# Kernel optimization log

Measured on AMD Instinct MI355X. Metric: run time of the kernel, lower is better.

Reference implementation:

```python
import jax, jax.numpy as jnp
import numpy as np

B, S, A, H, Z = 256, 512, 64, 1024, 256

def setup_inputs() -> dict:
    key = jax.random.key(0)
    ks = jax.random.split(key, 24)
    w = lambda k, shape: (jax.random.normal(k, shape, jnp.float32) * 0.02)
    inp = {
        "x": jax.random.randint(ks[0], (B, S), 0, A),
        "h0": jax.random.normal(ks[1], (B, H), jnp.float32),            # init_hidden randn
        "eps": jax.random.normal(ks[2], (S + 1, B, Z), jnp.float32),     # reparam noise per step + final
        "phi_x_w": w(ks[3], (H, A)),  "phi_x_b": jnp.zeros((H,), jnp.float32),
        "enc_w1": w(ks[4], (H, 2 * H)), "enc_b1": jnp.zeros((H,), jnp.float32),
        "enc_w2": w(ks[5], (Z, H)),     "enc_b2": jnp.zeros((Z,), jnp.float32),
        "pri_w1": w(ks[6], (H, H)),     "pri_b1": jnp.zeros((H,), jnp.float32),
        "pri_w2": w(ks[7], (Z, H)),     "pri_b2": jnp.zeros((Z,), jnp.float32),
        "phi_z_w": w(ks[8], (H, Z)),    "phi_z_b": jnp.zeros((H,), jnp.float32),
        "dec_w": w(ks[9], (H, 2 * H)),  "dec_b": jnp.zeros((H,), jnp.float32),
        "act_w": w(ks[10], (A, H)),     "act_b": jnp.zeros((A,), jnp.float32),
        "gru_wih": w(ks[11], (3 * H, 2 * H)), "gru_whh": w(ks[12], (3 * H, H)),
        "gru_bih": jnp.zeros((3 * H,), jnp.float32), "gru_bhh": jnp.zeros((3 * H,), jnp.float32),
    }
    return inp

def reference(x, h0, eps, phi_x_w, phi_x_b, enc_w1, enc_b1, enc_w2, enc_b2,
              pri_w1, pri_b1, pri_w2, pri_b2, phi_z_w, phi_z_b, dec_w, dec_b,
              act_w, act_b, gru_wih, gru_whh, gru_bih, gru_bhh):
    relu, sp = jax.nn.relu, jax.nn.softplus

    def gru_cell(xin, h):  # PyTorch GRU gate math
        gi = xin @ gru_wih.T + gru_bih
        gh = h @ gru_whh.T + gru_bhh
        ir, iz, inn = jnp.split(gi, 3, axis=-1)
        hr, hz, hn = jnp.split(gh, 3, axis=-1)
        r = jax.nn.sigmoid(ir + hr)
        zg = jax.nn.sigmoid(iz + hz)
        n = jnp.tanh(inn + r * hn)
        return (1.0 - zg) * n + zg * h

    def prior(h):
        p = relu(h @ pri_w1.T + pri_b1) @ pri_w2.T + pri_b2
        return p, sp(p)

    x_oh = jax.nn.one_hot(x, A, dtype=jnp.float32).transpose(1, 0, 2)  # [S,B,A]

    def step(carry, inp):
        h, kld = carry
        x_t, eps_t = inp
        px = relu(x_t @ phi_x_w.T + phi_x_b)                            # [B,H]
        enc = relu(jnp.concatenate([px, h], -1) @ enc_w1.T + enc_b1) @ enc_w2.T + enc_b2
        enc_std = sp(enc)
        pri_m, pri_std = prior(h)
        kld_el = (2 * jnp.log(pri_std) - 2 * jnp.log(enc_std)
                  + (enc_std ** 2 + (enc - pri_m) ** 2) / pri_std ** 2 - 1.0)
        kld = kld + 0.5 * jnp.sum(kld_el)
        z_t = eps_t * enc_std + enc                                     # reparam sample
        pz = relu(z_t @ phi_z_w.T + phi_z_b)
        h_new = gru_cell(jnp.concatenate([px, pz], -1), h)
        return (h_new, kld), None

    (h, kld), _ = jax.lax.scan(step, (h0, jnp.float32(0.0)), (x_oh, eps[:S]))

    pri_m, pri_std = prior(h)
    z_t = eps[S] * pri_std + pri_m
    pz = relu(z_t @ phi_z_w.T + phi_z_b)
    dec = relu(jnp.concatenate([pz, h], -1) @ dec_w.T + dec_b)
    pred_act = dec @ act_w.T + act_b
    return pred_act, kld
```

## Files before the change

### kernel.cpp

```cpp
#include <hip/hip_runtime.h>


typedef float f32x4 __attribute__((ext_vector_type(4)));
typedef __bf16 bf16x8 __attribute__((ext_vector_type(8)));
typedef unsigned long long u64;
typedef u64 u64x2 __attribute__((ext_vector_type(2)));

#define BB 256
#define SS 512
#define HH 1024
#define ZZ 256
#define AA 64
#define NWG 256

__device__ __forceinline__ float softplus_(float x) {
    return (x > 15.f) ? x : log1pf(expf(x));
}
__device__ __forceinline__ float sigmoid_(float x) {
    return 1.f / (1.f + expf(-x));
}

__device__ __forceinline__ u64 ld8a(const __bf16* p) {
    return __hip_atomic_load((const u64*)p, __ATOMIC_RELAXED, __HIP_MEMORY_SCOPE_AGENT);
}
__device__ __forceinline__ bf16x8 ld16a(const __bf16* p) {
    u64x2 t; t.x = ld8a(p); t.y = ld8a(p + 4);
    return __builtin_bit_cast(bf16x8, t);
}
__device__ __forceinline__ void st2a(__bf16* p, float v) {
    unsigned w = __builtin_bit_cast(unsigned short, (__bf16)v);
    asm volatile("global_store_short %0, %1, off sc0 sc1" :: "v"(p), "v"(w) : "memory");
}

__device__ __forceinline__ void gbarR(unsigned* bar, unsigned p, int wg) {
    __syncthreads();
    if (threadIdx.x == 0) {
        unsigned s = p & 7u;
        unsigned exp = (p >> 3) + 1u;
        unsigned* leaf = bar + (s * 8 + (wg >> 5)) * 16;
        unsigned* root = bar + (64 + s) * 16;
        unsigned* flag = bar + (72 + s) * 16;
        unsigned old = __hip_atomic_fetch_add(leaf, 1u, __ATOMIC_RELAXED, __HIP_MEMORY_SCOPE_AGENT);
        if (old == 32u * exp - 1u) {
            unsigned old2 = __hip_atomic_fetch_add(root, 1u, __ATOMIC_RELAXED, __HIP_MEMORY_SCOPE_AGENT);
            if (old2 == 8u * exp - 1u)
                __hip_atomic_store(flag, exp, __ATOMIC_RELAXED, __HIP_MEMORY_SCOPE_AGENT);
        }
        while (__hip_atomic_load(flag, __ATOMIC_RELAXED, __HIP_MEMORY_SCOPE_AGENT) < exp)
            __builtin_amdgcn_s_sleep(2);
    }
    asm volatile("buffer_inv sc0" ::: "memory");
    __syncthreads();
}

__device__ __forceinline__ void xbar(unsigned* flags, int g, int rank, int ngrp,
                                     unsigned tok) {
    __syncthreads();
    if (threadIdx.x == 0)
        __hip_atomic_store(flags + g * 256 + rank, tok, __ATOMIC_RELAXED,
                           __HIP_MEMORY_SCOPE_AGENT);
    unsigned l = threadIdx.x & 63;
    unsigned* base = flags + g * 256;
    for (;;) {
        bool ok = true;
        for (int i = (int)l; i < ngrp; i += 64)
            ok &= (__hip_atomic_load(base + i, __ATOMIC_RELAXED,
                                     __HIP_MEMORY_SCOPE_AGENT) >= tok);
        if (__all(ok)) break;
        __builtin_amdgcn_s_sleep(2);
    }
    asm volatile("buffer_inv sc0" ::: "memory");
    __syncthreads();
}

template<int MT, int NT>
__device__ __forceinline__ void wgemm(const __bf16* __restrict__ A, int lda, int mstride,
                                      const __bf16* __restrict__ B, int ldb, int nstride,
                                      int K, f32x4 (&acc)[MT][NT]) {
    int lane = threadIdx.x & 63;
    int rr = lane & 15;
    int ko = (lane >> 4) * 8;
    const __bf16* ap = A + rr * lda + ko;
    const __bf16* bp = B + rr * ldb + ko;
    #pragma unroll 2
    for (int k = 0; k < K; k += 32) {
        bf16x8 af[MT], bfr[NT];
        #pragma unroll
        for (int mt = 0; mt < MT; mt++) af[mt] = *(const bf16x8*)(ap + mt * mstride + k);
        #pragma unroll
        for (int nt = 0; nt < NT; nt++) bfr[nt] = *(const bf16x8*)(bp + nt * nstride + k);
        #pragma unroll
        for (int mt = 0; mt < MT; mt++)
            #pragma unroll
            for (int nt = 0; nt < NT; nt++)
                acc[mt][nt] = __builtin_amdgcn_mfma_f32_16x16x32_bf16(af[mt], bfr[nt], acc[mt][nt], 0, 0, 0);
    }
}


__global__ void k_zeroctl(unsigned* bar, unsigned* flags, unsigned* cnt, float* kldacc) {
    for (int i = threadIdx.x; i < 1280; i += 256) bar[i] = 0u;
    for (int i = threadIdx.x; i < 2048; i += 256) flags[i] = 0u;
    if (threadIdx.x < 8) cnt[threadIdx.x] = 0u;
    if (threadIdx.x == 0) *kldacc = 0.f;
}

__global__ void k_pack(const float* __restrict__ src, int src_ld, int col_off,
                       __bf16* __restrict__ dst, int cols, int total) {
    int i = blockIdx.x * 256 + threadIdx.x;
    if (i >= total) return;
    int r = i / cols, c = i - r * cols;
    dst[i] = (__bf16)src[r * src_ld + col_off + c];
}

__global__ void k_copyf(const float* __restrict__ s, float* __restrict__ d, int n) {
    int i = blockIdx.x * 256 + threadIdx.x;
    if (i < n) d[i] = s[i];
}

__global__ void k_px(const float* __restrict__ phi_x_w, const float* __restrict__ phi_x_b,
                     float* __restrict__ px) {
    int i = blockIdx.x * 256 + threadIdx.x;
    int a = i >> 10, hh = i & 1023;
    px[i] = fmaxf(phi_x_w[hh * AA + a] + phi_x_b[hh], 0.f);
}

__global__ __launch_bounds__(256) void k_tables(const float* __restrict__ enc_w1,
                                                const float* __restrict__ wih,
                                                const float* __restrict__ px,
                                                float* __restrict__ encpx,
                                                float* __restrict__ gipx) {
    __shared__ float spx[64][65];
    int tid = threadIdx.x;
    int cg = blockIdx.x * 4 + (tid >> 6);
    int a = tid & 63;
    const float* wrow = (cg < 1024) ? (enc_w1 + cg * 2048) : (wih + (cg - 1024) * 2048);
    float sum = 0.f;
    for (int k0 = 0; k0 < 1024; k0 += 64) {
        __syncthreads();
        for (int e = tid; e < 4096; e += 256)
            spx[e >> 6][e & 63] = px[((e >> 6) << 10) + k0 + (e & 63)];
        __syncthreads();
        #pragma unroll 8
        for (int kk = 0; kk < 64; kk++) sum += wrow[k0 + kk] * spx[a][kk];
    }
    if (cg < 1024) encpx[a * 1024 + cg] = sum;
    else gipx[a * 3072 + (cg - 1024)] = sum;
}


struct PArgs {
    const int* x; const float* eps;
    const __bf16 *WA, *W2, *WPZ, *WIH, *WHH, *WDEC, *WACT;
    const float *encpx, *gipx;
    const float *eb1, *pb1, *eb2, *pb2, *pzb, *decb, *actb, *bih, *bhh;
    float *hf0, *hf1; __bf16 *hb0, *hb1;
    __bf16 *hidcat, *zbuf, *pzbuf, *tailhid, *decbuf;
    float *gh; float *kldacc; unsigned *bar, *flags, *cnt;
    float* out;
};

__global__ __launch_bounds__(256, 1) void k_persist(PArgs a) {
    int wg = blockIdx.x;
    int tid = threadIdx.x;
    int v = tid >> 6;
    int lane = tid & 63;
    int rr = lane & 15;
    int ko = (lane >> 4) * 8;
    int col = lane & 15, rq = (lane >> 4) * 4;
    float kl = 0.f;
    float* hf[2] = {a.hf0, a.hf1};
    __bf16* hb[2] = {a.hb0, a.hb1};

    __shared__ __align__(16) __bf16 Alds[16][1032];
    __shared__ float lds2[4][2][256];
    __shared__ int sh_g, sh_rank, sh_ngrp;
    __shared__ float sh_kl[4];

    if (tid == 0) {
        unsigned xcc = __builtin_amdgcn_s_getreg((31 << 11) | (0 << 6) | 20) & 7u;
        sh_g = (int)xcc;
        sh_rank = (int)atomicAdd(a.cnt + xcc, 1u);
    }
    __syncthreads();
    int g = sh_g, rank = sh_rank;
    gbarR(a.bar, 0, wg);
    if (tid == 0)
        sh_ngrp = (int)__hip_atomic_load(a.cnt + g, __ATOMIC_RELAXED,
                                         __HIP_MEMORY_SCOPE_AGENT);
    __syncthreads();
    int ngrp = sh_ngrp;
    int base_m = g * 32;

    unsigned gp = 1;

    for (int t = 0; t < SS; t++) {
        int cur = t & 1, nxt = cur ^ 1;

        for (int r0 = rank; r0 < 32; r0 += ngrp) {
            int mt = r0 & 15;
            __syncthreads();
            {
                const __bf16* src = hb[cur] + (size_t)(mt * 16) * HH + tid * 4;
                u64 tmp[16];
                #pragma unroll
                for (int e2 = 0; e2 < 16; e2++) tmp[e2] = ld8a(src + (size_t)e2 * HH);
                #pragma unroll
                for (int e2 = 0; e2 < 16; e2++)
                    *(u64*)((char*)(&Alds[e2][0]) + tid * 8) = tmp[e2];
            }
            __syncthreads();
            int ntg = (r0 >> 4) + 2 * v;
            const __bf16* bp[5]; int qv[5];
            #pragma unroll
            for (int j = 0; j < 5; j++) {
                int q = ntg * 5 + j; qv[j] = q;
                const __bf16* b;
                if (q < 16) b = a.WA + (size_t)(g * 256 + q * 16 + rr) * HH;
                else {
                    int qq = q - 16;
                    b = a.WHH + (size_t)((qq >> 3) * 1024 + g * 128 + (qq & 7) * 16 + rr) * HH;
                }
                bp[j] = b + ko;
            }
            f32x4 acc[5] = {};
            const __bf16* arow = &Alds[rr][ko];
            #pragma unroll 4
            for (int k = 0; k < HH; k += 32) {
                bf16x8 af = *(const bf16x8*)(arow + k);
                #pragma unroll
                for (int j = 0; j < 5; j++)
                    acc[j] = __builtin_amdgcn_mfma_f32_16x16x32_bf16(
                        af, *(const bf16x8*)(bp[j] + k), acc[j], 0, 0, 0);
            }
            int xb[4];
            #pragma unroll
            for (int i = 0; i < 4; i++) xb[i] = a.x[(mt * 16 + rq + i) * SS + t];
            #pragma unroll
            for (int j = 0; j < 5; j++) {
                int q = qv[j];
                if (q < 16) {
                    int c = g * 256 + q * 16 + col;
                    if (c < 1024) {
                        float bias = a.eb1[c];
                        #pragma unroll
                        for (int i = 0; i < 4; i++) {
                            int m = mt * 16 + rq + i;
                            float val = acc[j][i] + bias + a.encpx[xb[i] * 1024 + c];
                            st2a(&a.hidcat[(size_t)m * 2048 + c], fmaxf(val, 0.f));
                        }
                    } else {
                        float bias = a.pb1[c - 1024];
                        #pragma unroll
                        for (int i = 0; i < 4; i++) {
                            int m = mt * 16 + rq + i;
                            st2a(&a.hidcat[(size_t)m * 2048 + c], fmaxf(acc[j][i] + bias, 0.f));
                        }
                    }
                } else {
                    int qq = q - 16;
                    int gc = (qq >> 3) * 1024 + g * 128 + (qq & 7) * 16 + col;
                    #pragma unroll
                    for (int i = 0; i < 4; i++)
                        a.gh[(size_t)(mt * 16 + rq + i) * 3072 + gc] = acc[j][i];
                }
            }
        }
        gbarR(a.bar, gp++, wg);

        for (int r = rank; r < 32; r += ngrp) {
            int mtl = r >> 1;
            int zsl = g * 2 + (r & 1);
            const __bf16* ae_p = a.hidcat + (size_t)(mtl * 16 + rr) * 2048 + v * 256 + ko;
            const __bf16* ap_p = ae_p + 1024;
            const __bf16* be_p = a.W2 + (size_t)(zsl * 16 + rr) * HH + v * 256 + ko;
            const __bf16* bp_p = a.W2 + (size_t)(256 + zsl * 16 + rr) * HH + v * 256 + ko;
            bf16x8 aef[8], apf[8];
            #pragma unroll
            for (int k8 = 0; k8 < 8; k8++) {
                aef[k8] = ld16a(ae_p + k8 * 32);
                apf[k8] = ld16a(ap_p + k8 * 32);
            }
            f32x4 ae = {0.f,0.f,0.f,0.f}, av = {0.f,0.f,0.f,0.f};
            #pragma unroll
            for (int k8 = 0; k8 < 8; k8++) {
                ae = __builtin_amdgcn_mfma_f32_16x16x32_bf16(
                    aef[k8], *(const bf16x8*)(be_p + k8 * 32), ae, 0, 0, 0);
                av = __builtin_amdgcn_mfma_f32_16x16x32_bf16(
                    apf[k8], *(const bf16x8*)(bp_p + k8 * 32), av, 0, 0, 0);
            }
            #pragma unroll
            for (int i = 0; i < 4; i++) {
                int idx = (rq + i) * 16 + col;
                lds2[v][0][idx] = ae[i];
                lds2[v][1][idx] = av[i];
            }
            __syncthreads();
            {
                float e = lds2[0][0][tid] + lds2[1][0][tid] + lds2[2][0][tid] + lds2[3][0][tid];
                float pv = lds2[0][1][tid] + lds2[1][1][tid] + lds2[2][1][tid] + lds2[3][1][tid];
                int m = mtl * 16 + (tid >> 4);
                int z = zsl * 16 + (tid & 15);
                float enc = e + a.eb2[z];
                float pri = pv + a.pb2[z];
                float es = softplus_(enc), ps = softplus_(pri);
                float d = enc - pri;
                kl += 2.f * (logf(ps) - logf(es)) + (es * es + d * d) / (ps * ps) - 1.f;
                const float* epst = a.eps + (size_t)t * BB * ZZ;
                st2a(&a.zbuf[(size_t)m * ZZ + z], epst[m * ZZ + z] * es + enc);
            }
            __syncthreads();
        }
        gbarR(a.bar, gp++, wg);

        for (int r0 = rank; r0 < 32; r0 += ngrp) {
            int mt = r0 & 15;
            int nt = (r0 >> 4) + 2 * v;
            const __bf16* apz = a.zbuf + (size_t)(mt * 16 + rr) * ZZ + ko;
            const __bf16* bpz = a.WPZ + (size_t)((g * 8 + nt) * 16 + rr) * ZZ + ko;
            bf16x8 azf[8];
            #pragma unroll
            for (int k8 = 0; k8 < 8; k8++) azf[k8] = ld16a(apz + k8 * 32);
            f32x4 acc = {0.f,0.f,0.f,0.f};
            #pragma unroll
            for (int k8 = 0; k8 < 8; k8++)
                acc = __builtin_amdgcn_mfma_f32_16x16x32_bf16(
                    azf[k8], *(const bf16x8*)(bpz + k8 * 32), acc, 0, 0, 0);
            int n = (g * 8 + nt) * 16 + col;
            float b = a.pzb[n];
            #pragma unroll
            for (int i = 0; i < 4; i++)
                st2a(&a.pzbuf[(size_t)(mt * 16 + rq + i) * HH + n], fmaxf(acc[i] + b, 0.f));
        }
        gbarR(a.bar, gp++, wg);

        for (int r0 = rank; r0 < 32; r0 += ngrp) {
            int mt = r0 & 15;
            __syncthreads();
            {
                const __bf16* src = a.pzbuf + (size_t)(mt * 16) * HH + tid * 4;
                u64 tmp[16];
                #pragma unroll
                for (int e2 = 0; e2 < 16; e2++) tmp[e2] = ld8a(src + (size_t)e2 * HH);
                #pragma unroll
                for (int e2 = 0; e2 < 16; e2++)
                    *(u64*)((char*)(&Alds[e2][0]) + tid * 8) = tmp[e2];
            }
            __syncthreads();
            int jt = (r0 >> 4) + 2 * v;
            int jtg = g * 8 + jt;
            const __bf16* bp0 = a.WIH + (size_t)(jtg * 16 + rr) * HH + ko;
            const __bf16* bp1g = bp0 + (size_t)1024 * HH;
            const __bf16* bp2g = bp0 + (size_t)2048 * HH;
            f32x4 acc[3] = {};
            const __bf16* arow = &Alds[rr][ko];
            #pragma unroll 4
            for (int k = 0; k < HH; k += 32) {
                bf16x8 af = *(const bf16x8*)(arow + k);
                acc[0] = __builtin_amdgcn_mfma_f32_16x16x32_bf16(af, *(const bf16x8*)(bp0 + k), acc[0], 0, 0, 0);
                acc[1] = __builtin_amdgcn_mfma_f32_16x16x32_bf16(af, *(const bf16x8*)(bp1g + k), acc[1], 0, 0, 0);
                acc[2] = __builtin_amdgcn_mfma_f32_16x16x32_bf16(af, *(const bf16x8*)(bp2g + k), acc[2], 0, 0, 0);
            }
            int j = jtg * 16 + col;
            float br = a.bih[j], bz2 = a.bih[1024 + j], bn = a.bih[2048 + j];
            float cr = a.bhh[j], cz = a.bhh[1024 + j], cn = a.bhh[2048 + j];
            #pragma unroll
            for (int i = 0; i < 4; i++) {
                int m = mt * 16 + rq + i;
                int xb = a.x[m * SS + t];
                const float* gpp = a.gipx + (size_t)xb * 3072;
                const float* ghrow = a.gh + (size_t)m * 3072;
                float gir = acc[0][i] + gpp[j] + br;
                float giz = acc[1][i] + gpp[1024 + j] + bz2;
                float gin = acc[2][i] + gpp[2048 + j] + bn;
                float ghr = ghrow[j] + cr;
                float ghz = ghrow[1024 + j] + cz;
                float ghn = ghrow[2048 + j] + cn;
                float rg = sigmoid_(gir + ghr);
                float zg = sigmoid_(giz + ghz);
                float nn = tanhf(gin + rg * ghn);
                float hv2 = (1.f - zg) * nn + zg * hf[cur][(size_t)m * HH + j];
                hf[nxt][(size_t)m * HH + j] = hv2;
                st2a(&hb[nxt][(size_t)m * HH + j], hv2);
            }
        }
        gbarR(a.bar, gp++, wg);
    }

    unsigned tok = 1;
    for (int r = rank; r < 32; r += ngrp) {
        int mt = v >> 1, nt = r * 2 + (v & 1);
        f32x4 acc[1][1] = {};
        wgemm<1, 1>(hb[0] + (size_t)(base_m + mt * 16) * HH, HH, 0,
                    a.WA + (size_t)(1024 + nt * 16) * HH, HH, 0, HH, acc);
        int n = nt * 16 + col;
        float b = a.pb1[n];
        #pragma unroll
        for (int i = 0; i < 4; i++) {
            int m = base_m + mt * 16 + rq + i;
            a.tailhid[m * HH + n] = (__bf16)fmaxf(acc[0][0][i] + b, 0.f);
        }
    }
    xbar(a.flags, g, rank, ngrp, tok++);
    if (v == 0) {
        for (int r = rank; r < 32; r += ngrp) {
            int mtl = r >> 4, zt = r & 15;
            f32x4 apv[1][1] = {};
            wgemm<1, 1>(a.tailhid + (size_t)(base_m + mtl * 16) * HH, HH, 0,
                        a.W2 + (size_t)(256 + zt * 16) * HH, HH, 0, HH, apv);
            int z = zt * 16 + col;
            float bp = a.pb2[z];
            const float* epst = a.eps + (size_t)SS * BB * ZZ;
            #pragma unroll
            for (int i = 0; i < 4; i++) {
                int m = base_m + mtl * 16 + rq + i;
                float pri = apv[0][0][i] + bp;
                float ps = softplus_(pri);
                a.zbuf[m * ZZ + z] = (__bf16)(epst[m * ZZ + z] * ps + pri);
            }
        }
    }
    xbar(a.flags, g, rank, ngrp, tok++);
    for (int r = rank; r < 32; r += ngrp) {
        int mt = v >> 1, nt = r * 2 + (v & 1);
        f32x4 acc[1][1] = {};
        wgemm<1, 1>(a.zbuf + (size_t)(base_m + mt * 16) * ZZ, ZZ, 0,
                    a.WPZ + (size_t)(nt * 16) * ZZ, ZZ, 0, ZZ, acc);
        int n = nt * 16 + col;
        float b = a.pzb[n];
        #pragma unroll
        for (int i = 0; i < 4; i++) {
            int m = base_m + mt * 16 + rq + i;
            a.pzbuf[m * HH + n] = (__bf16)fmaxf(acc[0][0][i] + b, 0.f);
        }
    }
    xbar(a.flags, g, rank, ngrp, tok++);
    for (int r = rank; r < 32; r += ngrp) {
        int mt = v >> 1, nt = r * 2 + (v & 1);
        f32x4 acc[1][1] = {};
        wgemm<1, 1>(a.pzbuf + (size_t)(base_m + mt * 16) * HH, HH, 0,
                    a.WDEC + (size_t)(nt * 16) * 2048, 2048, 0, HH, acc);
        wgemm<1, 1>(hb[0] + (size_t)(base_m + mt * 16) * HH, HH, 0,
                    a.WDEC + (size_t)(nt * 16) * 2048 + 1024, 2048, 0, HH, acc);
        int n = nt * 16 + col;
        float b = a.decb[n];
        #pragma unroll
        for (int i = 0; i < 4; i++) {
            int m = base_m + mt * 16 + rq + i;
            a.decbuf[m * HH + n] = (__bf16)fmaxf(acc[0][0][i] + b, 0.f);
        }
    }
    xbar(a.flags, g, rank, ngrp, tok++);
    if (v == 0) {
        for (int r = rank; r < 32; r += ngrp) {
            if (r >= 8) continue;
            int mt = r >> 2, nt = r & 3;
            f32x4 acc[1][1] = {};
            wgemm<1, 1>(a.decbuf + (size_t)(base_m + mt * 16) * HH, HH, 0,
                        a.WACT + (size_t)(nt * 16) * HH, HH, 0, HH, acc);
            int n = nt * 16 + col;
            float b = a.actb[n];
            #pragma unroll
            for (int i = 0; i < 4; i++) {
                int m = base_m + mt * 16 + rq + i;
                a.out[m * AA + n] = acc[0][0][i] + b;
            }
        }
    }

    {
        float s = kl;
        #pragma unroll
        for (int off = 1; off < 64; off <<= 1) s += __shfl_xor(s, off);
        if (lane == 0) sh_kl[v] = s;
        __syncthreads();
        if (tid == 0) {
            float ws = sh_kl[0] + sh_kl[1] + sh_kl[2] + sh_kl[3];
            atomicAdd(a.kldacc, ws);
        }
    }
    gbarR(a.bar, gp++, wg);
    if (wg == 0 && tid == 0) {
        float s = __hip_atomic_load(a.kldacc, __ATOMIC_ACQUIRE, __HIP_MEMORY_SCOPE_AGENT);
        a.out[BB * AA] = 0.5f * s;
    }
}

extern "C" void kernel_launch(void* const* d_in, const int* in_sizes, int n_in,
                              void* d_out, int out_size, void* d_ws, size_t ws_size,
                              hipStream_t stream) {
    const int*   x       = (const int*)d_in[0];
    const float* h0      = (const float*)d_in[1];
    const float* eps     = (const float*)d_in[2];
    const float* phi_x_w = (const float*)d_in[3];
    const float* phi_x_b = (const float*)d_in[4];
    const float* enc_w1  = (const float*)d_in[5];
    const float* enc_b1  = (const float*)d_in[6];
    const float* enc_w2  = (const float*)d_in[7];
    const float* enc_b2  = (const float*)d_in[8];
    const float* pri_w1  = (const float*)d_in[9];
    const float* pri_b1  = (const float*)d_in[10];
    const float* pri_w2  = (const float*)d_in[11];
    const float* pri_b2  = (const float*)d_in[12];
    const float* phi_z_w = (const float*)d_in[13];
    const float* phi_z_b = (const float*)d_in[14];
    const float* dec_w   = (const float*)d_in[15];
    const float* dec_b   = (const float*)d_in[16];
    const float* act_w   = (const float*)d_in[17];
    const float* act_b   = (const float*)d_in[18];
    const float* gru_wih = (const float*)d_in[19];
    const float* gru_whh = (const float*)d_in[20];
    const float* gru_bih = (const float*)d_in[21];
    const float* gru_bhh = (const float*)d_in[22];

    char* p = (char*)d_ws;
    auto alloc = [&](size_t bytes) { char* r = p; p += (bytes + 255) & ~(size_t)255; return r; };

    __bf16* WA    = (__bf16*)alloc(2048 * 1024 * 2);
    __bf16* W2    = (__bf16*)alloc(512 * 1024 * 2);
    __bf16* WPZ   = (__bf16*)alloc(1024 * 256 * 2);
    __bf16* WIH   = (__bf16*)alloc(3072 * 1024 * 2);
    __bf16* WHH   = (__bf16*)alloc(3072 * 1024 * 2);
    __bf16* WDEC  = (__bf16*)alloc(1024 * 2048 * 2);
    __bf16* WACT  = (__bf16*)alloc(64 * 1024 * 2);
    float*  px    = (float*)alloc(64 * 1024 * 4);
    float*  encpx = (float*)alloc(64 * 1024 * 4);
    float*  gipx  = (float*)alloc(64 * 3072 * 4);
    float*  hf0   = (float*)alloc(BB * HH * 4);
    float*  hf1   = (float*)alloc(BB * HH * 4);
    __bf16* hb0   = (__bf16*)alloc(BB * HH * 2);
    __bf16* hb1   = (__bf16*)alloc(BB * HH * 2);
    __bf16* hidcat = (__bf16*)alloc(BB * 2048 * 2);
    __bf16* zbuf   = (__bf16*)alloc(BB * ZZ * 2);
    __bf16* pzbuf  = (__bf16*)alloc(BB * HH * 2);
    __bf16* tailhid = (__bf16*)alloc(BB * HH * 2);
    __bf16* decbuf  = (__bf16*)alloc(BB * HH * 2);
    float*  gh     = (float*)alloc(BB * 3072 * 4);
    unsigned* bar  = (unsigned*)alloc(1280 * 4);
    unsigned* flags = (unsigned*)alloc(2048 * 4);
    unsigned* cnt  = (unsigned*)alloc(64 * 4);
    float*  kldacc = (float*)alloc(256);

    auto pack = [&](const float* src, int src_ld, int off, __bf16* dst, int rows, int cols) {
        int total = rows * cols;
        k_pack<<<(total + 255) / 256, 256, 0, stream>>>(src, src_ld, off, dst, cols, total);
    };

    k_zeroctl<<<1, 256, 0, stream>>>(bar, flags, cnt, kldacc);
    pack(enc_w1, 2048, 1024, WA, 1024, 1024);
    pack(pri_w1, 1024, 0, WA + 1024 * 1024, 1024, 1024);
    pack(enc_w2, 1024, 0, W2, 256, 1024);
    pack(pri_w2, 1024, 0, W2 + 256 * 1024, 256, 1024);
    pack(phi_z_w, 256, 0, WPZ, 1024, 256);
    pack(gru_wih, 2048, 1024, WIH, 3072, 1024);
    pack(gru_whh, 1024, 0, WHH, 3072, 1024);
    pack(dec_w, 2048, 0, WDEC, 1024, 2048);
    pack(act_w, 1024, 0, WACT, 64, 1024);
    pack(h0, 1024, 0, hb0, 256, 1024);
    k_copyf<<<(BB * HH + 255) / 256, 256, 0, stream>>>(h0, hf0, BB * HH);
    k_px<<<(64 * 1024) / 256, 256, 0, stream>>>(phi_x_w, phi_x_b, px);
    k_tables<<<1024, 256, 0, stream>>>(enc_w1, gru_wih, px, encpx, gipx);

    PArgs pa;
    pa.x = x; pa.eps = eps;
    pa.WA = WA; pa.W2 = W2; pa.WPZ = WPZ; pa.WIH = WIH; pa.WHH = WHH;
    pa.WDEC = WDEC; pa.WACT = WACT;
    pa.encpx = encpx; pa.gipx = gipx;
    pa.eb1 = enc_b1; pa.pb1 = pri_b1; pa.eb2 = enc_b2; pa.pb2 = pri_b2;
    pa.pzb = phi_z_b; pa.decb = dec_b; pa.actb = act_b;
    pa.bih = gru_bih; pa.bhh = gru_bhh;
    pa.hf0 = hf0; pa.hf1 = hf1; pa.hb0 = hb0; pa.hb1 = hb1;
    pa.hidcat = hidcat; pa.zbuf = zbuf; pa.pzbuf = pzbuf;
    pa.tailhid = tailhid; pa.decbuf = decbuf;
    pa.gh = gh; pa.kldacc = kldacc;
    pa.bar = bar; pa.flags = flags; pa.cnt = cnt;
    pa.out = (float*)d_out;

    k_persist<<<dim3(NWG), dim3(256), 0, stream>>>(pa);
}
```

Baseline: 32.39 ms.

## Replace two grid barriers per step with per-XCD group barriers via redundant local compute

Each XCD group now computes the full encoder-mean projection and reparameterized z for all latent columns into a group-local buffer, then the phi_z layer into a group-local pz buffer. This replaces two of the four grid-wide barriers per timestep with cheaper intra-XCD flag barriers. The grid barrier release now writes a separate flag per XCD to avoid contention on one line. Epilogues are also transposed to write packed 4-wide bf16/f32 stores instead of scalar short stores. The cost is redundant GEMM work (enc_w2 and phi_z computed eight times) and more memory for the per-group buffers.

```diff
diff --git a/kernel.cpp b/kernel.cpp
--- a/kernel.cpp
+++ b/kernel.cpp
@@ -4,7 +4,6 @@
 typedef float f32x4 __attribute__((ext_vector_type(4)));
 typedef __bf16 bf16x8 __attribute__((ext_vector_type(8)));
 typedef unsigned long long u64;
-typedef u64 u64x2 __attribute__((ext_vector_type(2)));
 
 #define BB 256
 #define SS 512
@@ -12,6 +11,7 @@
 #define ZZ 256
 #define AA 64
 #define NWG 256
+#define MFMA __builtin_amdgcn_mfma_f32_16x16x32_bf16
 
 __device__ __forceinline__ float softplus_(float x) {
     return (x > 15.f) ? x : log1pf(expf(x));
@@ -20,31 +20,36 @@
     return 1.f / (1.f + expf(-x));
 }
 
-__device__ __forceinline__ u64 ld8a(const __bf16* p) {
+__device__ __forceinline__ u64 ld8a(const void* p) {
     return __hip_atomic_load((const u64*)p, __ATOMIC_RELAXED, __HIP_MEMORY_SCOPE_AGENT);
 }
-__device__ __forceinline__ bf16x8 ld16a(const __bf16* p) {
-    u64x2 t; t.x = ld8a(p); t.y = ld8a(p + 4);
-    return __builtin_bit_cast(bf16x8, t);
-}
-__device__ __forceinline__ void st2a(__bf16* p, float v) {
-    unsigned w = __builtin_bit_cast(unsigned short, (__bf16)v);
-    asm volatile("global_store_short %0, %1, off sc0 sc1" :: "v"(p), "v"(w) : "memory");
-}
-
-__device__ __forceinline__ void gbarR(unsigned* bar, unsigned p, int wg) {
+__device__ __forceinline__ void st8a(void* p, u64 v) {
+    __hip_atomic_store((u64*)p, v, __ATOMIC_RELAXED, __HIP_MEMORY_SCOPE_AGENT);
+}
+__device__ __forceinline__ u64 pack4bf(float a0, float a1, float a2, float a3) {
+    union { __bf16 h[4]; u64 w; } pk;
+    pk.h[0] = (__bf16)a0; pk.h[1] = (__bf16)a1;
+    pk.h[2] = (__bf16)a2; pk.h[3] = (__bf16)a3;
+    return pk.w;
+}
+
+__device__ __forceinline__ void gbarG(unsigned* bar, unsigned p, int wg, int g) {
     __syncthreads();
     if (threadIdx.x == 0) {
         unsigned s = p & 7u;
         unsigned exp = (p >> 3) + 1u;
         unsigned* leaf = bar + (s * 8 + (wg >> 5)) * 16;
         unsigned* root = bar + (64 + s) * 16;
-        unsigned* flag = bar + (72 + s) * 16;
+        unsigned* flag = bar + (128 + (s * 8 + g)) * 16;
         unsigned old = __hip_atomic_fetch_add(leaf, 1u, __ATOMIC_RELAXED, __HIP_MEMORY_SCOPE_AGENT);
         if (old == 32u * exp - 1u) {
             unsigned old2 = __hip_atomic_fetch_add(root, 1u, __ATOMIC_RELAXED, __HIP_MEMORY_SCOPE_AGENT);
-            if (old2 == 8u * exp - 1u)
-                __hip_atomic_store(flag, exp, __ATOMIC_RELAXED, __HIP_MEMORY_SCOPE_AGENT);
+            if (old2 == 8u * exp - 1u) {
+                #pragma unroll
+                for (int gg = 0; gg < 8; gg++)
+                    __hip_atomic_store(bar + (128 + (s * 8 + gg)) * 16, exp,
+                                       __ATOMIC_RELAXED, __HIP_MEMORY_SCOPE_AGENT);
+            }
         }
         while (__hip_atomic_load(flag, __ATOMIC_RELAXED, __HIP_MEMORY_SCOPE_AGENT) < exp)
             __builtin_amdgcn_s_sleep(2);
@@ -93,13 +98,13 @@
         for (int mt = 0; mt < MT; mt++)
             #pragma unroll
             for (int nt = 0; nt < NT; nt++)
-                acc[mt][nt] = __builtin_amdgcn_mfma_f32_16x16x32_bf16(af[mt], bfr[nt], acc[mt][nt], 0, 0, 0);
+                acc[mt][nt] = MFMA(af[mt], bfr[nt], acc[mt][nt], 0, 0, 0);
     }
 }
 
 
 __global__ void k_zeroctl(unsigned* bar, unsigned* flags, unsigned* cnt, float* kldacc) {
-    for (int i = threadIdx.x; i < 1280; i += 256) bar[i] = 0u;
+    for (int i = threadIdx.x; i < 4096; i += 256) bar[i] = 0u;
     for (int i = threadIdx.x; i < 2048; i += 256) flags[i] = 0u;
     if (threadIdx.x < 8) cnt[threadIdx.x] = 0u;
     if (threadIdx.x == 0) *kldacc = 0.f;
@@ -156,6 +161,7 @@
     const float *eb1, *pb1, *eb2, *pb2, *pzb, *decb, *actb, *bih, *bhh;
     float *hf0, *hf1; __bf16 *hb0, *hb1;
     __bf16 *hidcat, *zbuf, *pzbuf, *tailhid, *decbuf;
+    __bf16 *zloc8, *pzloc8;
     float *gh; float *kldacc; unsigned *bar, *flags, *cnt;
     float* out;
 };
@@ -167,13 +173,13 @@
     int lane = tid & 63;
     int rr = lane & 15;
     int ko = (lane >> 4) * 8;
-    int col = lane & 15, rq = (lane >> 4) * 4;
+    int col = lane & 15;
+    int rq = (lane >> 4) * 4;
     float kl = 0.f;
     float* hf[2] = {a.hf0, a.hf1};
     __bf16* hb[2] = {a.hb0, a.hb1};
 
-    __shared__ __align__(16) __bf16 Alds[16][1032];
-    __shared__ float lds2[4][2][256];
+    __shared__ __align__(16) __bf16 Alds[16][2056];
     __shared__ int sh_g, sh_rank, sh_ngrp;
     __shared__ float sh_kl[4];
 
@@ -184,33 +190,35 @@
     }
     __syncthreads();
     int g = sh_g, rank = sh_rank;
-    gbarR(a.bar, 0, wg);
+    gbarG(a.bar, 0, wg, g);
     if (tid == 0)
         sh_ngrp = (int)__hip_atomic_load(a.cnt + g, __ATOMIC_RELAXED,
                                          __HIP_MEMORY_SCOPE_AGENT);
     __syncthreads();
     int ngrp = sh_ngrp;
     int base_m = g * 32;
+    __bf16* zloc = a.zloc8 + (size_t)g * BB * ZZ;
+    __bf16* pzloc = a.pzloc8 + (size_t)g * BB * HH;
 
     unsigned gp = 1;
+    unsigned tok = 1;
 
     for (int t = 0; t < SS; t++) {
         int cur = t & 1, nxt = cur ^ 1;
 
         for (int r0 = rank; r0 < 32; r0 += ngrp) {
-            int mt = r0 & 15;
+            int mt = r0 & 15, half = r0 >> 4;
             __syncthreads();
             {
                 const __bf16* src = hb[cur] + (size_t)(mt * 16) * HH + tid * 4;
                 u64 tmp[16];
                 #pragma unroll
-                for (int e2 = 0; e2 < 16; e2++) tmp[e2] = ld8a(src + (size_t)e2 * HH);
-                #pragma unroll
-                for (int e2 = 0; e2 < 16; e2++)
-                    *(u64*)((char*)(&Alds[e2][0]) + tid * 8) = tmp[e2];
+                for (int e = 0; e < 16; e++) tmp[e] = ld8a(src + (size_t)e * HH);
+                #pragma unroll
+                for (int e = 0; e < 16; e++) *(u64*)(&Alds[e][tid * 4]) = tmp[e];
             }
             __syncthreads();
-            int ntg = (r0 >> 4) + 2 * v;
+            int ntg = half * 4 + v;
             const __bf16* bp[5]; int qv[5];
             #pragma unroll
             for (int j = 0; j < 5; j++) {
@@ -230,125 +238,145 @@
                 bf16x8 af = *(const bf16x8*)(arow + k);
                 #pragma unroll
                 for (int j = 0; j < 5; j++)
-                    acc[j] = __builtin_amdgcn_mfma_f32_16x16x32_bf16(
-                        af, *(const bf16x8*)(bp[j] + k), acc[j], 0, 0, 0);
-            }
-            int xb[4];
-            #pragma unroll
-            for (int i = 0; i < 4; i++) xb[i] = a.x[(mt * 16 + rq + i) * SS + t];
+                    acc[j] = MFMA(*(const bf16x8*)(bp[j] + k), af, acc[j], 0, 0, 0);
+            }
+            int m = mt * 16 + col;
             #pragma unroll
             for (int j = 0; j < 5; j++) {
                 int q = qv[j];
                 if (q < 16) {
-                    int c = g * 256 + q * 16 + col;
+                    int c = g * 256 + q * 16 + rq;
                     if (c < 1024) {
-                        float bias = a.eb1[c];
-                        #pragma unroll
-                        for (int i = 0; i < 4; i++) {
-                            int m = mt * 16 + rq + i;
-                            float val = acc[j][i] + bias + a.encpx[xb[i] * 1024 + c];
-                            st2a(&a.hidcat[(size_t)m * 2048 + c], fmaxf(val, 0.f));
-                        }
+                        int xb = a.x[m * SS + t];
+                        f32x4 bias = *(const f32x4*)(a.eb1 + c);
+                        f32x4 ep = *(const f32x4*)(a.encpx + (size_t)xb * 1024 + c);
+                        st8a(&a.hidcat[(size_t)m * 2048 + c],
+                             pack4bf(fmaxf(acc[j][0] + bias[0] + ep[0], 0.f),
+                                     fmaxf(acc[j][1] + bias[1] + ep[1], 0.f),
+                                     fmaxf(acc[j][2] + bias[2] + ep[2], 0.f),
+                                     fmaxf(acc[j][3] + bias[3] + ep[3], 0.f)));
                     } else {
-                        float bias = a.pb1[c - 1024];
-                        #pragma unroll
-                        for (int i = 0; i < 4; i++) {
-                            int m = mt * 16 + rq + i;
-                            st2a(&a.hidcat[(size_t)m * 2048 + c], fmaxf(acc[j][i] + bias, 0.f));
-                        }
+                        f32x4 bias = *(const f32x4*)(a.pb1 + (c - 1024));
+                        st8a(&a.hidcat[(size_t)m * 2048 + c],
+                             pack4bf(fmaxf(acc[j][0] + bias[0], 0.f),
+                                     fmaxf(acc[j][1] + bias[1], 0.f),
+                                     fmaxf(acc[j][2] + bias[2], 0.f),
+                                     fmaxf(acc[j][3] + bias[3], 0.f)));
                     }
                 } else {
                     int qq = q - 16;
-                    int gc = (qq >> 3) * 1024 + g * 128 + (qq & 7) * 16 + col;
-                    #pragma unroll
-                    for (int i = 0; i < 4; i++)
-                        a.gh[(size_t)(mt * 16 + rq + i) * 3072 + gc] = acc[j][i];
+                    int gc = (qq >> 3) * 1024 + g * 128 + (qq & 7) * 16 + rq;
+                    f32x4 w = {acc[j][0], acc[j][1], acc[j][2], acc[j][3]};
+                    *(f32x4*)(a.gh + (size_t)m * 3072 + gc) = w;
                 }
             }
         }
-        gbarR(a.bar, gp++, wg);
-
-        for (int r = rank; r < 32; r += ngrp) {
-            int mtl = r >> 1;
-            int zsl = g * 2 + (r & 1);
-            const __bf16* ae_p = a.hidcat + (size_t)(mtl * 16 + rr) * 2048 + v * 256 + ko;
-            const __bf16* ap_p = ae_p + 1024;
-            const __bf16* be_p = a.W2 + (size_t)(zsl * 16 + rr) * HH + v * 256 + ko;
-            const __bf16* bp_p = a.W2 + (size_t)(256 + zsl * 16 + rr) * HH + v * 256 + ko;
-            bf16x8 aef[8], apf[8];
-            #pragma unroll
-            for (int k8 = 0; k8 < 8; k8++) {
-                aef[k8] = ld16a(ae_p + k8 * 32);
-                apf[k8] = ld16a(ap_p + k8 * 32);
-            }
-            f32x4 ae = {0.f,0.f,0.f,0.f}, av = {0.f,0.f,0.f,0.f};
-            #pragma unroll
-            for (int k8 = 0; k8 < 8; k8++) {
-                ae = __builtin_amdgcn_mfma_f32_16x16x32_bf16(
-                    aef[k8], *(const bf16x8*)(be_p + k8 * 32), ae, 0, 0, 0);
-                av = __builtin_amdgcn_mfma_f32_16x16x32_bf16(
-                    apf[k8], *(const bf16x8*)(bp_p + k8 * 32), av, 0, 0, 0);
-            }
-            #pragma unroll
-            for (int i = 0; i < 4; i++) {
-                int idx = (rq + i) * 16 + col;
-                lds2[v][0][idx] = ae[i];
-                lds2[v][1][idx] = av[i];
-            }
+        gbarG(a.bar, gp++, wg, g);
+
+        for (int r0 = rank; r0 < 32; r0 += ngrp) {
+            int mt = r0 & 15, zh = r0 >> 4;
             __syncthreads();
             {
-                float e = lds2[0][0][tid] + lds2[1][0][tid] + lds2[2][0][tid] + lds2[3][0][tid];
-                float pv = lds2[0][1][tid] + lds2[1][1][tid] + lds2[2][1][tid] + lds2[3][1][tid];
-                int m = mtl * 16 + (tid >> 4);
-                int z = zsl * 16 + (tid & 15);
-                float enc = e + a.eb2[z];
-                float pri = pv + a.pb2[z];
-                float es = softplus_(enc), ps = softplus_(pri);
-                float d = enc - pri;
-                kl += 2.f * (logf(ps) - logf(es)) + (es * es + d * d) / (ps * ps) - 1.f;
-                const float* epst = a.eps + (size_t)t * BB * ZZ;
-                st2a(&a.zbuf[(size_t)m * ZZ + z], epst[m * ZZ + z] * es + enc);
+                const __bf16* src = a.hidcat + (size_t)(mt * 16) * 2048 + tid * 4;
+                u64 t0[16], t1[16];
+                #pragma unroll
+                for (int e = 0; e < 16; e++) t0[e] = ld8a(src + (size_t)e * 2048);
+                #pragma unroll
+                for (int e = 0; e < 16; e++) t1[e] = ld8a(src + 1024 + (size_t)e * 2048);
+                #pragma unroll
+                for (int e = 0; e < 16; e++) {
+                    *(u64*)(&Alds[e][tid * 4]) = t0[e];
+                    *(u64*)(&Alds[e][1024 + tid * 4]) = t1[e];
+                }
             }
             __syncthreads();
-        }
-        gbarR(a.bar, gp++, wg);
+            const __bf16* arow = &Alds[rr][ko];
+            #pragma unroll
+            for (int zz = 0; zz < 2; zz++) {
+                int zt = zh * 8 + v * 2 + zz;
+                const __bf16* be = a.W2 + (size_t)(zt * 16 + rr) * HH + ko;
+                f32x4 ae = {0.f, 0.f, 0.f, 0.f};
+                #pragma unroll 4
+                for (int k = 0; k < HH; k += 32)
+                    ae = MFMA(*(const bf16x8*)(be + k), *(const bf16x8*)(arow + k), ae, 0, 0, 0);
+                int m = mt * 16 + col;
+                int z = zt * 16 + rq;
+                f32x4 b_e = *(const f32x4*)(a.eb2 + z);
+                const float* epst = a.eps + (size_t)t * BB * ZZ + (size_t)m * ZZ + z;
+                union { u64 w; float f[2]; } u0, u1;
+                u0.w = ld8a(epst); u1.w = ld8a(epst + 2);
+                float ef[4] = {u0.f[0], u0.f[1], u1.f[0], u1.f[1]};
+                float enc[4], es[4];
+                #pragma unroll
+                for (int i = 0; i < 4; i++) {
+                    enc[i] = ae[i] + b_e[i];
+                    es[i] = softplus_(enc[i]);
+                }
+                if ((zt >> 1) == g) {
+                    const __bf16* bpr = a.W2 + (size_t)(256 + zt * 16 + rr) * HH + ko;
+                    f32x4 av = {0.f, 0.f, 0.f, 0.f};
+                    #pragma unroll 4
+                    for (int k = 0; k < HH; k += 32)
+                        av = MFMA(*(const bf16x8*)(bpr + k),
+                                  *(const bf16x8*)(arow + 1024 + k), av, 0, 0, 0);
+                    f32x4 b_p = *(const f32x4*)(a.pb2 + z);
+                    #pragma unroll
+                    for (int i = 0; i < 4; i++) {
+                        float pri = av[i] + b_p[i];
+                        float ps = softplus_(pri);
+                        float d = enc[i] - pri;
+                        kl += 2.f * (logf(ps) - logf(es[i]))
+                              + (es[i] * es[i] + d * d) / (ps * ps) - 1.f;
+                    }
+                }
+                *(u64*)(zloc + (size_t)m * ZZ + z) =
+                    pack4bf(ef[0] * es[0] + enc[0], ef[1] * es[1] + enc[1],
+                            ef[2] * es[2] + enc[2], ef[3] * es[3] + enc[3]);
+            }
+        }
+        xbar(a.flags, g, rank, ngrp, tok++);
 
         for (int r0 = rank; r0 < 32; r0 += ngrp) {
-            int mt = r0 & 15;
-            int nt = (r0 >> 4) + 2 * v;
-            const __bf16* apz = a.zbuf + (size_t)(mt * 16 + rr) * ZZ + ko;
-            const __bf16* bpz = a.WPZ + (size_t)((g * 8 + nt) * 16 + rr) * ZZ + ko;
-            bf16x8 azf[8];
-            #pragma unroll
-            for (int k8 = 0; k8 < 8; k8++) azf[k8] = ld16a(apz + k8 * 32);
-            f32x4 acc = {0.f,0.f,0.f,0.f};
-            #pragma unroll
-            for (int k8 = 0; k8 < 8; k8++)
-                acc = __builtin_amdgcn_mfma_f32_16x16x32_bf16(
-                    azf[k8], *(const bf16x8*)(bpz + k8 * 32), acc, 0, 0, 0);
-            int n = (g * 8 + nt) * 16 + col;
-            float b = a.pzb[n];
-            #pragma unroll
-            for (int i = 0; i < 4; i++)
-                st2a(&a.pzbuf[(size_t)(mt * 16 + rq + i) * HH + n], fmaxf(acc[i] + b, 0.f));
-        }
-        gbarR(a.bar, gp++, wg);
+            int mt = r0 & 15, nh = r0 >> 4;
+            const __bf16* az = zloc + (size_t)(mt * 16 + rr) * ZZ + ko;
+            int nt0 = nh * 32 + v * 8;
+            const __bf16* bwz[8];
+            #pragma unroll
+            for (int j = 0; j < 8; j++)
+                bwz[j] = a.WPZ + (size_t)((nt0 + j) * 16 + rr) * ZZ + ko;
+            f32x4 acc[8] = {};
+            #pragma unroll
+            for (int k = 0; k < ZZ; k += 32) {
+                bf16x8 af = *(const bf16x8*)(az + k);
+                #pragma unroll
+                for (int j = 0; j < 8; j++)
+                    acc[j] = MFMA(*(const bf16x8*)(bwz[j] + k), af, acc[j], 0, 0, 0);
+            }
+            int m = mt * 16 + col;
+            #pragma unroll
+            for (int j = 0; j < 8; j++) {
+                int n = (nt0 + j) * 16 + rq;
+                f32x4 bb = *(const f32x4*)(a.pzb + n);
+                *(u64*)(pzloc + (size_t)m * HH + n) =
+                    pack4bf(fmaxf(acc[j][0] + bb[0], 0.f), fmaxf(acc[j][1] + bb[1], 0.f),
+                            fmaxf(acc[j][2] + bb[2], 0.f), fmaxf(acc[j][3] + bb[3], 0.f));
+            }
+        }
+        xbar(a.flags, g, rank, ngrp, tok++);
 
         for (int r0 = rank; r0 < 32; r0 += ngrp) {
-            int mt = r0 & 15;
+            int mt = r0 & 15, jh = r0 >> 4;
             __syncthreads();
             {
-                const __bf16* src = a.pzbuf + (size_t)(mt * 16) * HH + tid * 4;
+                const __bf16* src = pzloc + (size_t)(mt * 16) * HH + tid * 4;
                 u64 tmp[16];
                 #pragma unroll
-                for (int e2 = 0; e2 < 16; e2++) tmp[e2] = ld8a(src + (size_t)e2 * HH);
-                #pragma unroll
-                for (int e2 = 0; e2 < 16; e2++)
-                    *(u64*)((char*)(&Alds[e2][0]) + tid * 8) = tmp[e2];
+                for (int e = 0; e < 16; e++) tmp[e] = *(const u64*)(src + (size_t)e * HH);
+                #pragma unroll
+                for (int e = 0; e < 16; e++) *(u64*)(&Alds[e][tid * 4]) = tmp[e];
             }
             __syncthreads();
-            int jt = (r0 >> 4) + 2 * v;
-            int jtg = g * 8 + jt;
+            int jtg = g * 8 + jh * 4 + v;
             const __bf16* bp0 = a.WIH + (size_t)(jtg * 16 + rr) * HH + ko;
             const __bf16* bp1g = bp0 + (size_t)1024 * HH;
             const __bf16* bp2g = bp0 + (size_t)2048 * HH;
@@ -357,37 +385,49 @@
             #pragma unroll 4
             for (int k = 0; k < HH; k += 32) {
                 bf16x8 af = *(const bf16x8*)(arow + k);
-                acc[0] = __builtin_amdgcn_mfma_f32_16x16x32_bf16(af, *(const bf16x8*)(bp0 + k), acc[0], 0, 0, 0);
-                acc[1] = __builtin_amdgcn_mfma_f32_16x16x32_bf16(af, *(const bf16x8*)(bp1g + k), acc[1], 0, 0, 0);
-                acc[2] = __builtin_amdgcn_mfma_f32_16x16x32_bf16(af, *(const bf16x8*)(bp2g + k), acc[2], 0, 0, 0);
-            }
-            int j = jtg * 16 + col;
-            float br = a.bih[j], bz2 = a.bih[1024 + j], bn = a.bih[2048 + j];
-            float cr = a.bhh[j], cz = a.bhh[1024 + j], cn = a.bhh[2048 + j];
+                acc[0] = MFMA(*(const bf16x8*)(bp0 + k), af, acc[0], 0, 0, 0);
+                acc[1] = MFMA(*(const bf16x8*)(bp1g + k), af, acc[1], 0, 0, 0);
+                acc[2] = MFMA(*(const bf16x8*)(bp2g + k), af, acc[2], 0, 0, 0);
+            }
+            int m = mt * 16 + col;
+            int j = jtg * 16 + rq;
+            int xb = a.x[m * SS + t];
+            const float* gpb = a.gipx + (size_t)xb * 3072;
+            f32x4 gp0 = *(const f32x4*)(gpb + j);
+            f32x4 gp1 = *(const f32x4*)(gpb + 1024 + j);
+            f32x4 gp2 = *(const f32x4*)(gpb + 2048 + j);
+            f32x4 br = *(const f32x4*)(a.bih + j);
+            f32x4 bz4 = *(const f32x4*)(a.bih + 1024 + j);
+            f32x4 bn4 = *(const f32x4*)(a.bih + 2048 + j);
+            f32x4 cr = *(const f32x4*)(a.bhh + j);
+            f32x4 cz = *(const f32x4*)(a.bhh + 1024 + j);
+            f32x4 cn = *(const f32x4*)(a.bhh + 2048 + j);
+            const float* ghrow = a.gh + (size_t)m * 3072;
+            f32x4 gh0 = *(const f32x4*)(ghrow + j);
+            f32x4 gh1 = *(const f32x4*)(ghrow + 1024 + j);
+            f32x4 gh2 = *(const f32x4*)(ghrow + 2048 + j);
+            f32x4 hcur = *(const f32x4*)(hf[cur] + (size_t)m * HH + j);
+            float hv[4];
             #pragma unroll
             for (int i = 0; i < 4; i++) {
-                int m = mt * 16 + rq + i;
-                int xb = a.x[m * SS + t];
-                const float* gpp = a.gipx + (size_t)xb * 3072;
-                const float* ghrow = a.gh + (size_t)m * 3072;
-                float gir = acc[0][i] + gpp[j] + br;
-                float giz = acc[1][i] + gpp[1024 + j] + bz2;
-                float gin = acc[2][i] + gpp[2048 + j] + bn;
-                float ghr = ghrow[j] + cr;
-                float ghz = ghrow[1024 + j] + cz;
-                float ghn = ghrow[2048 + j] + cn;
+                float gir = acc[0][i] + gp0[i] + br[i];
+                float giz = acc[1][i] + gp1[i] + bz4[i];
+                float gin = acc[2][i] + gp2[i] + bn4[i];
+                float ghr = gh0[i] + cr[i];
+                float ghz = gh1[i] + cz[i];
+                float ghn = gh2[i] + cn[i];
                 float rg = sigmoid_(gir + ghr);
                 float zg = sigmoid_(giz + ghz);
                 float nn = tanhf(gin + rg * ghn);
-                float hv2 = (1.f - zg) * nn + zg * hf[cur][(size_t)m * HH + j];
-                hf[nxt][(size_t)m * HH + j] = hv2;
-                st2a(&hb[nxt][(size_t)m * HH + j], hv2);
-            }
-        }
-        gbarR(a.bar, gp++, wg);
-    }
-
-    unsigned tok = 1;
+                hv[i] = (1.f - zg) * nn + zg * hcur[i];
+            }
+            f32x4 hw = {hv[0], hv[1], hv[2], hv[3]};
+            *(f32x4*)(hf[nxt] + (size_t)m * HH + j) = hw;
+            st8a(&hb[nxt][(size_t)m * HH + j], pack4bf(hv[0], hv[1], hv[2], hv[3]));
+        }
+        gbarG(a.bar, gp++, wg, g);
+    }
+
     for (int r = rank; r < 32; r += ngrp) {
         int mt = v >> 1, nt = r * 2 + (v & 1);
         f32x4 acc[1][1] = {};
@@ -479,7 +519,7 @@
             atomicAdd(a.kldacc, ws);
         }
     }
-    gbarR(a.bar, gp++, wg);
+    gbarG(a.bar, gp++, wg, g);
     if (wg == 0 && tid == 0) {
         float s = __hip_atomic_load(a.kldacc, __ATOMIC_ACQUIRE, __HIP_MEMORY_SCOPE_AGENT);
         a.out[BB * AA] = 0.5f * s;
@@ -535,8 +575,10 @@
     __bf16* pzbuf  = (__bf16*)alloc(BB * HH * 2);
     __bf16* tailhid = (__bf16*)alloc(BB * HH * 2);
     __bf16* decbuf  = (__bf16*)alloc(BB * HH * 2);
+    __bf16* zloc8  = (__bf16*)alloc((size_t)8 * BB * ZZ * 2);
+    __bf16* pzloc8 = (__bf16*)alloc((size_t)8 * BB * HH * 2);
     float*  gh     = (float*)alloc(BB * 3072 * 4);
-    unsigned* bar  = (unsigned*)alloc(1280 * 4);
+    unsigned* bar  = (unsigned*)alloc(4096 * 4);
     unsigned* flags = (unsigned*)alloc(2048 * 4);
     unsigned* cnt  = (unsigned*)alloc(64 * 4);
     float*  kldacc = (float*)alloc(256);
@@ -572,6 +614,7 @@
     pa.hf0 = hf0; pa.hf1 = hf1; pa.hb0 = hb0; pa.hb1 = hb1;
     pa.hidcat = hidcat; pa.zbuf = zbuf; pa.pzbuf = pzbuf;
     pa.tailhid = tailhid; pa.decbuf = decbuf;
+    pa.zloc8 = zloc8; pa.pzloc8 = pzloc8;
     pa.gh = gh; pa.kldacc = kldacc;
     pa.bar = bar; pa.flags = flags; pa.cnt = cnt;
     pa.out = (float*)d_out;
```

New measurement: 41.25 ms. 1.27x slower.
